# Kernel tuning notes

Measured on AMD Instinct MI355X. Metric: run time of the kernel, lower is better.

The kernel has to match this reference:

```python
import jax, jax.numpy as jnp
import numpy as np
import math

LOG2 = math.log(2.0)

def shifted_softplus(x):
    return jax.nn.softplus(x) - LOG2

def setup_inputs() -> dict:
    key = jax.random.key(0)
    ks = jax.random.split(key, 12)
    n_atoms, n_pairs = 40000, 640000
    d_basis, d_filt, n_rbf = 128, 128, 20
    x = jax.random.normal(ks[0], (n_atoms, d_basis), dtype=jnp.float32)
    f_ij = jax.random.uniform(ks[1], (n_pairs, n_rbf), dtype=jnp.float32)
    idx_i = jax.random.randint(ks[2], (n_pairs,), 0, n_atoms)
    idx_j = jax.random.randint(ks[3], (n_pairs,), 0, n_atoms)
    rcut_ij = jax.random.uniform(ks[4], (n_pairs,), dtype=jnp.float32)
    s_in = 1.0 / math.sqrt(d_basis)
    s_f = 1.0 / math.sqrt(n_rbf)
    s_out = 1.0 / math.sqrt(d_filt)
    W_in = jax.random.uniform(ks[5], (d_filt, d_basis), minval=-s_in, maxval=s_in)
    b_in = jax.random.uniform(ks[6], (d_filt,), minval=-s_in, maxval=s_in)
    W_f = jax.random.uniform(ks[7], (d_filt, n_rbf), minval=-s_f, maxval=s_f)
    b_f = jax.random.uniform(ks[8], (d_filt,), minval=-s_f, maxval=s_f)
    W_out = jax.random.uniform(ks[9], (d_basis, d_filt), minval=-s_out, maxval=s_out)
    b_out = jax.random.uniform(ks[10], (d_basis,), minval=-s_out, maxval=s_out)
    return {"x": x, "f_ij": f_ij, "idx_i": idx_i, "idx_j": idx_j, "rcut_ij": rcut_ij,
            "W_in": W_in, "b_in": b_in, "W_f": W_f, "b_f": b_f, "W_out": W_out, "b_out": b_out}

def reference(x, f_ij, idx_i, idx_j, rcut_ij, W_in, b_in, W_f, b_f, W_out, b_out):
    n_atoms = x.shape[0]
    # input_to_feature: Linear(d_basis -> d_filt)
    h = x @ W_in.T + b_in                                  # [n_atoms, d_filt]
    # filter_network: Linear(n_rbf -> d_filt) + ShiftedSoftplus, scaled by cutoff
    Wij = shifted_softplus(f_ij @ W_f.T + b_f) * rcut_ij[:, None]  # [n_pairs, d_filt]
    # gather neighbor features, modulate, scatter-add back to atoms
    x_ij = h[idx_j] * Wij                                  # [n_pairs, d_filt]
    agg = jax.ops.segment_sum(x_ij, idx_i, num_segments=n_atoms)   # [n_atoms, d_filt]
    # feature_to_output: Linear(d_filt -> d_basis) + ShiftedSoftplus
    return shifted_softplus(agg @ W_out.T + b_out)
```

## Files before the change

### kernel.cpp

```cpp
#include <hip/hip_runtime.h>
#include <hip/hip_bf16.h>
#include <hip/hip_fp16.h>

typedef __hip_bfloat16 bf16;
typedef __attribute__((ext_vector_type(8))) short short8;
typedef __attribute__((ext_vector_type(4))) float f32x4;

__device__ __forceinline__ float braw2f(unsigned short u) {
    return __uint_as_float(((unsigned int)u) << 16);
}
__device__ __forceinline__ unsigned short f2braw(float f) {
    bf16 b = __float2bfloat16(f);
    return *(unsigned short*)&b;
}
__device__ __forceinline__ unsigned int pack2(float lo, float hi) {
    return (unsigned int)f2braw(lo) | ((unsigned int)f2braw(hi) << 16);
}
__device__ __forceinline__ float h2f(unsigned short u) {
    __half h = *(__half*)&u;
    return __half2float(h);
}

#define LN2F 0.69314718055994531f
__device__ __forceinline__ float ssp(float x) {
    return fmaxf(x, 0.0f) + __logf(1.0f + __expf(-fabsf(x))) - LN2F;
}

template<bool ACT, bool OUT_BF16>
__global__ __launch_bounds__(256) void linear128_mfma_kernel(
    const float* __restrict__ X, const float* __restrict__ W, const float* __restrict__ Bias,
    void* __restrict__ Yv, int n_rows)
{
    __shared__ unsigned short wls[128 * 128];
    __shared__ unsigned short xs[64 * 128];
    __shared__ float bls[128];

    const float4* W4 = (const float4*)W;
    for (int i = threadIdx.x; i < 128 * 32; i += 256) {
        float4 w = W4[i];
        ushort4 s; s.x = f2braw(w.x); s.y = f2braw(w.y); s.z = f2braw(w.z); s.w = f2braw(w.w);
        *(ushort4*)&wls[i * 4] = s;
    }
    if (threadIdx.x < 128) bls[threadIdx.x] = Bias[threadIdx.x];

    const int base = blockIdx.x * 64;
    const float4* X4 = (const float4*)X;
    for (int i = threadIdx.x; i < 64 * 32; i += 256) {
        int r = i >> 5, k4 = i & 31;
        int row = base + r;
        float4 v = (row < n_rows) ? X4[(size_t)row * 32 + k4] : make_float4(0.f, 0.f, 0.f, 0.f);
        ushort4 s; s.x = f2braw(v.x); s.y = f2braw(v.y); s.z = f2braw(v.z); s.w = f2braw(v.w);
        *(ushort4*)&xs[r * 128 + k4 * 4] = s;
    }
    __syncthreads();

    const int wv = threadIdx.x >> 6;
    const int l  = threadIdx.x & 63;
    const int lm = l & 15;
    const int lq = l >> 4;

    short8 a[4];
    #pragma unroll
    for (int kk = 0; kk < 4; ++kk)
        a[kk] = *(const short8*)&xs[(wv * 16 + lm) * 128 + kk * 32 + lq * 8];

    f32x4 acc[8];
    #pragma unroll
    for (int ct = 0; ct < 8; ++ct) {
        f32x4 c = {0.f, 0.f, 0.f, 0.f};
        #pragma unroll
        for (int kk = 0; kk < 4; ++kk) {
            short8 b = *(const short8*)&wls[(ct * 16 + lm) * 128 + kk * 32 + lq * 8];
            c = __builtin_amdgcn_mfma_f32_16x16x32_bf16(a[kk], b, c, 0, 0, 0);
        }
        acc[ct] = c;
    }

    #pragma unroll
    for (int ct = 0; ct < 8; ++ct) {
        int col = ct * 16 + lm;
        float bia = bls[col];
        #pragma unroll
        for (int r = 0; r < 4; ++r) {
            int row = base + wv * 16 + lq * 4 + r;
            if (row < n_rows) {
                float o = acc[ct][r] + bia;
                if (ACT) o = ssp(o);
                if (OUT_BF16) ((unsigned short*)Yv)[(size_t)row * 128 + col] = f2braw(o);
                else          ((float*)Yv)[(size_t)row * 128 + col] = o;
            }
        }
    }
}


__global__ __launch_bounds__(256) void zero_int_kernel(int* __restrict__ p, int n) {
    int i = blockIdx.x * 256 + threadIdx.x;
    if (i < n) p[i] = 0;
}

__global__ __launch_bounds__(256) void hist_kernel(
    const int* __restrict__ idx_i, int* __restrict__ cnt, int n_pairs, int n_atoms)
{
    for (int p = blockIdx.x * 256 + threadIdx.x; p < n_pairs; p += gridDim.x * 256) {
        int ai = idx_i[p];
        if ((unsigned)ai < (unsigned)n_atoms) atomicAdd(&cnt[ai], 1);
    }
}

__global__ __launch_bounds__(1024) void scan1_kernel(
    const int* __restrict__ cnt, int* __restrict__ offs, int* __restrict__ partials, int n)
{
    __shared__ int sm[1024];
    int t = threadIdx.x, idx = blockIdx.x * 1024 + t;
    int v = (idx < n) ? cnt[idx] : 0;
    sm[t] = v;
    __syncthreads();
    #pragma unroll
    for (int d = 1; d < 1024; d <<= 1) {
        int tmp = (t >= d) ? sm[t - d] : 0;
        __syncthreads();
        sm[t] += tmp;
        __syncthreads();
    }
    if (idx < n) offs[idx] = sm[t] - v;
    if (t == 1023) partials[blockIdx.x] = sm[1023];
}

__global__ __launch_bounds__(64) void scan2_kernel(
    int* __restrict__ partials, int* __restrict__ offs, int nb, int n)
{
    __shared__ int sm[64];
    int t = threadIdx.x;
    int v = (t < nb) ? partials[t] : 0;
    sm[t] = v;
    __syncthreads();
    #pragma unroll
    for (int d = 1; d < 64; d <<= 1) {
        int tmp = (t >= d) ? sm[t - d] : 0;
        __syncthreads();
        sm[t] += tmp;
        __syncthreads();
    }
    if (t < nb) partials[t] = sm[t] - v;
    if (t == 63) offs[n] = sm[63];
}

__global__ __launch_bounds__(1024) void scan3_kernel(
    int* __restrict__ offs, int* __restrict__ cur, const int* __restrict__ partials, int n)
{
    int idx = blockIdx.x * 1024 + threadIdx.x;
    if (idx < n) {
        int o = offs[idx] + partials[blockIdx.x];
        offs[idx] = o;
        cur[idx] = o;
    }
}

template<bool WRITE_ATOM>
__global__ __launch_bounds__(256) void scatter_pay_kernel(
    const float* __restrict__ f_ij, const int* __restrict__ idx_i, const int* __restrict__ idx_j,
    const float* __restrict__ rcut, int* __restrict__ cur, uint4* __restrict__ pay,
    int* __restrict__ pair_atom, int n_pairs, int n_atoms)
{
    if (blockIdx.x == 0 && threadIdx.x < 204) {
        ((int*)(pay + (size_t)n_pairs * 3))[threadIdx.x] = 0;
    }
    for (int p = blockIdx.x * 256 + threadIdx.x; p < n_pairs; p += gridDim.x * 256) {
        int ai = idx_i[p];
        if ((unsigned)ai >= (unsigned)n_atoms) continue;
        int pos = atomicAdd(&cur[ai], 1);
        const float4* fr = (const float4*)(f_ij + (size_t)p * 20);
        float4 f0 = fr[0], f1 = fr[1], f2 = fr[2], f3 = fr[3], f4 = fr[4];
        uint4 q0, q1, q2;
        q0.x = pack2(f0.x, f0.y); q0.y = pack2(f0.z, f0.w);
        q0.z = pack2(f1.x, f1.y); q0.w = pack2(f1.z, f1.w);
        q1.x = pack2(f2.x, f2.y); q1.y = pack2(f2.z, f2.w);
        q1.z = pack2(f3.x, f3.y); q1.w = pack2(f3.z, f3.w);
        q2.x = pack2(f4.x, f4.y); q2.y = pack2(f4.z, f4.w);
        q2.z = (unsigned int)idx_j[p];
        q2.w = __float_as_uint(rcut[p]);
        uint4* dst = pay + (size_t)pos * 3;
        dst[0] = q0; dst[1] = q1; dst[2] = q2;
        if (WRITE_ATOM) pair_atom[pos] = ai;
    }
}

__global__ __launch_bounds__(256) void fused_pair_kernel(
    const uint4* __restrict__ pay, const int* __restrict__ pair_atom,
    const float* __restrict__ W_f, const float* __restrict__ b_f,
    const unsigned int* __restrict__ hb32, float* __restrict__ agg, int n_pairs)
{
    __shared__ unsigned short wls[128 * 40];
    __shared__ float bls[128];
    __shared__ unsigned short wij[64 * 132];
    __shared__ int lds_atom[64];
    __shared__ int lds_aj[64];

    for (int i = threadIdx.x; i < 128 * 32; i += 256) {
        int col = i >> 5, k = i & 31;
        float v = (k < 20) ? W_f[col * 20 + k] : 0.f;
        wls[col * 40 + k] = f2braw(v);
    }
    if (threadIdx.x < 128) bls[threadIdx.x] = b_f[threadIdx.x];

    const int P0 = blockIdx.x * 64;
    if (threadIdx.x < 64) {
        int p = P0 + threadIdx.x;
        bool valid = p < n_pairs;
        lds_atom[threadIdx.x] = valid ? pair_atom[p] : -1;
        lds_aj[threadIdx.x]   = valid ? (int)((const unsigned int*)pay)[(size_t)p * 12 + 10] : 0;
    }
    __syncthreads();

    const int wv = threadIdx.x >> 6;
    const int l  = threadIdx.x & 63;
    const int lm = l & 15;
    const int lq = l >> 4;
    const int p0 = P0 + wv * 16;

    if (p0 < n_pairs) {
        const char* rec = (const char*)pay + (size_t)(p0 + lm) * 48;
        short8 a = *(const short8*)(rec + lq * 16);
        if (lq == 2) { a[4] = 0; a[5] = 0; a[6] = 0; a[7] = 0; }
        if (lq == 3) { a[0]=0; a[1]=0; a[2]=0; a[3]=0; a[4]=0; a[5]=0; a[6]=0; a[7]=0; }

        f32x4 acc[8];
        #pragma unroll
        for (int ct = 0; ct < 8; ++ct) {
            short8 b = *(const short8*)&wls[(ct * 16 + lm) * 40 + lq * 8];
            f32x4 z = {0.f, 0.f, 0.f, 0.f};
            acc[ct] = __builtin_amdgcn_mfma_f32_16x16x32_bf16(a, b, z, 0, 0, 0);
        }

        float rc[4];
        #pragma unroll
        for (int r = 0; r < 4; ++r) {
            int p = p0 + lq * 4 + r;
            rc[r] = (p < n_pairs) ? ((const float*)pay)[(size_t)p * 12 + 11] : 0.f;
        }
        #pragma unroll
        for (int ct = 0; ct < 8; ++ct) {
            float bia = bls[ct * 16 + lm];
            #pragma unroll
            for (int r = 0; r < 4; ++r) {
                float o = ssp(acc[ct][r] + bia) * rc[r];
                __half hh = __float2half(o);
                wij[(wv * 16 + lq * 4 + r) * 132 + ct * 16 + lm] = *(unsigned short*)&hh;
            }
        }
    }
    __syncthreads();

    int nv = n_pairs - p0;
    if (nv > 16) nv = 16;
    if (nv > 0) {
        float a0 = 0.f, a1 = 0.f;
        int cura = lds_atom[wv * 16];
        #pragma unroll 4
        for (int k = 0; k < nv; ++k) {
            int pa = lds_atom[wv * 16 + k];
            if (pa != cura) {
                atomicAdd(&agg[(size_t)cura * 128 + 2 * l], a0);
                atomicAdd(&agg[(size_t)cura * 128 + 2 * l + 1], a1);
                a0 = 0.f; a1 = 0.f; cura = pa;
            }
            int aj = lds_aj[wv * 16 + k];
            unsigned int h = hb32[(size_t)aj * 64 + l];
            unsigned int w = *(const unsigned int*)&wij[(wv * 16 + k) * 132 + 2 * l];
            a0 += __uint_as_float(h << 16) * h2f((unsigned short)(w & 0xffffu));
            a1 += __uint_as_float(h & 0xffff0000u) * h2f((unsigned short)(w >> 16));
        }
        atomicAdd(&agg[(size_t)cura * 128 + 2 * l], a0);
        atomicAdd(&agg[(size_t)cura * 128 + 2 * l + 1], a1);
    }
}

__global__ __launch_bounds__(256) void segment_pay_kernel(
    const uint4* __restrict__ pay, const float* __restrict__ W_f,
    const float* __restrict__ b_f, const unsigned int* __restrict__ hb32,
    const int* __restrict__ offs, float* __restrict__ agg, int n_atoms)
{
    const int wave = (blockIdx.x * 256 + threadIdx.x) >> 6;
    const int lane = threadIdx.x & 63;
    if (wave >= n_atoms) return;

    const int c0 = 2 * lane;
    float w0[20], w1[20];
    #pragma unroll
    for (int r = 0; r < 20; ++r) {
        w0[r] = W_f[c0 * 20 + r];
        w1[r] = W_f[(c0 + 1) * 20 + r];
    }
    const float b0 = b_f[c0], b1 = b_f[c0 + 1];

    const int cs = offs[wave], ce = offs[wave + 1];
    float acc0 = 0.f, acc1 = 0.f;

    int s = cs;
    for (; s + 2 <= ce; s += 2) {
        const uint4* pA = pay + (size_t)s * 3;
        const uint4* pB = pA + 3;
        uint4 qA0 = pA[0], qA1 = pA[1], qA2 = pA[2];
        uint4 qB0 = pB[0], qB1 = pB[1], qB2 = pB[2];
        unsigned int uA[10] = {qA0.x,qA0.y,qA0.z,qA0.w,qA1.x,qA1.y,qA1.z,qA1.w,qA2.x,qA2.y};
        unsigned int uB[10] = {qB0.x,qB0.y,qB0.z,qB0.w,qB1.x,qB1.y,qB1.z,qB1.w,qB2.x,qB2.y};
        float a0A = b0, a1A = b1, a0B = b0, a1B = b1;
        #pragma unroll
        for (int r = 0; r < 10; ++r) {
            float loA = __uint_as_float(uA[r] << 16);
            float hiA = __uint_as_float(uA[r] & 0xffff0000u);
            float loB = __uint_as_float(uB[r] << 16);
            float hiB = __uint_as_float(uB[r] & 0xffff0000u);
            a0A += loA * w0[2*r];     a1A += loA * w1[2*r];
            a0A += hiA * w0[2*r + 1]; a1A += hiA * w1[2*r + 1];
            a0B += loB * w0[2*r];     a1B += loB * w1[2*r];
            a0B += hiB * w0[2*r + 1]; a1B += hiB * w1[2*r + 1];
        }
        float rcA = __uint_as_float(qA2.w), rcB = __uint_as_float(qB2.w);
        float wv0A = ssp(a0A) * rcA, wv1A = ssp(a1A) * rcA;
        float wv0B = ssp(a0B) * rcB, wv1B = ssp(a1B) * rcB;
        unsigned int hA = hb32[(size_t)(int)qA2.z * 64 + lane];
        unsigned int hB = hb32[(size_t)(int)qB2.z * 64 + lane];
        acc0 += __uint_as_float(hA << 16) * wv0A + __uint_as_float(hB << 16) * wv0B;
        acc1 += __uint_as_float(hA & 0xffff0000u) * wv1A + __uint_as_float(hB & 0xffff0000u) * wv1B;
    }
    if (s < ce) {
        const uint4* pA = pay + (size_t)s * 3;
        uint4 q0 = pA[0], q1 = pA[1], q2 = pA[2];
        unsigned int u[10] = {q0.x,q0.y,q0.z,q0.w,q1.x,q1.y,q1.z,q1.w,q2.x,q2.y};
        float a0 = b0, a1 = b1;
        #pragma unroll
        for (int r = 0; r < 10; ++r) {
            float lo = __uint_as_float(u[r] << 16);
            float hi = __uint_as_float(u[r] & 0xffff0000u);
            a0 += lo * w0[2*r];     a1 += lo * w1[2*r];
            a0 += hi * w0[2*r + 1]; a1 += hi * w1[2*r + 1];
        }
        float rc = __uint_as_float(q2.w);
        float wv0 = ssp(a0) * rc, wv1 = ssp(a1) * rc;
        unsigned int h = hb32[(size_t)(int)q2.z * 64 + lane];
        acc0 += __uint_as_float(h << 16) * wv0;
        acc1 += __uint_as_float(h & 0xffff0000u) * wv1;
    }

    *(float2*)&agg[(size_t)wave * 128 + c0] = make_float2(acc0, acc1);
}

__global__ __launch_bounds__(256) void scatter_kernel(
    const int* __restrict__ idx_i, int* __restrict__ cur, int* __restrict__ perm,
    int n_pairs, int n_atoms)
{
    for (int p = blockIdx.x * 256 + threadIdx.x; p < n_pairs; p += gridDim.x * 256) {
        int ai = idx_i[p];
        if ((unsigned)ai < (unsigned)n_atoms) {
            int pos = atomicAdd(&cur[ai], 1);
            perm[pos] = p;
        }
    }
}

__global__ __launch_bounds__(256) void segment_kernel(
    const float* __restrict__ f_ij, const int* __restrict__ idx_j,
    const float* __restrict__ rcut, const float* __restrict__ W_f,
    const float* __restrict__ b_f, const unsigned short* __restrict__ hb,
    const int* __restrict__ offs, const int* __restrict__ perm,
    float* __restrict__ agg, int n_atoms)
{
    const int wave = (blockIdx.x * 256 + threadIdx.x) >> 6;
    const int lane = threadIdx.x & 63;
    if (wave >= n_atoms) return;

    float w0[20], w1[20];
    #pragma unroll
    for (int r = 0; r < 20; ++r) {
        w0[r] = W_f[lane * 20 + r];
        w1[r] = W_f[(lane + 64) * 20 + r];
    }
    const float b0 = b_f[lane], b1 = b_f[lane + 64];

    const int cs = offs[wave], ce = offs[wave + 1];
    float acc0 = 0.f, acc1 = 0.f;

    int s = cs;
    for (; s + 2 <= ce; s += 2) {
        int pA = perm[s], pB = perm[s + 1];
        int ajA = idx_j[pA], ajB = idx_j[pB];
        float rcA = rcut[pA], rcB = rcut[pB];
        const float4* frA = (const float4*)(f_ij + (size_t)pA * 20);
        const float4* frB = (const float4*)(f_ij + (size_t)pB * 20);
        float a0A = b0, a1A = b1, a0B = b0, a1B = b1;
        #pragma unroll
        for (int q = 0; q < 5; ++q) {
            float4 fA = frA[q], fB = frB[q];
            a0A += fA.x * w0[4*q+0]; a1A += fA.x * w1[4*q+0];
            a0A += fA.y * w0[4*q+1]; a1A += fA.y * w1[4*q+1];
            a0A += fA.z * w0[4*q+2]; a1A += fA.z * w1[4*q+2];
            a0A += fA.w * w0[4*q+3]; a1A += fA.w * w1[4*q+3];
            a0B += fB.x * w0[4*q+0]; a1B += fB.x * w1[4*q+0];
            a0B += fB.y * w0[4*q+1]; a1B += fB.y * w1[4*q+1];
            a0B += fB.z * w0[4*q+2]; a1B += fB.z * w1[4*q+2];
            a0B += fB.w * w0[4*q+3]; a1B += fB.w * w1[4*q+3];
        }
        float wv0A = ssp(a0A) * rcA, wv1A = ssp(a1A) * rcA;
        float wv0B = ssp(a0B) * rcB, wv1B = ssp(a1B) * rcB;
        float h0A = braw2f(hb[(size_t)ajA * 128 + lane]);
        float h1A = braw2f(hb[(size_t)ajA * 128 + 64 + lane]);
        float h0B = braw2f(hb[(size_t)ajB * 128 + lane]);
        float h1B = braw2f(hb[(size_t)ajB * 128 + 64 + lane]);
        acc0 += h0A * wv0A + h0B * wv0B;
        acc1 += h1A * wv1A + h1B * wv1B;
    }
    if (s < ce) {
        int p = perm[s];
        int aj = idx_j[p];
        float rc = rcut[p];
        const float4* fr = (const float4*)(f_ij + (size_t)p * 20);
        float a0 = b0, a1 = b1;
        #pragma unroll
        for (int q = 0; q < 5; ++q) {
            float4 fv = fr[q];
            a0 += fv.x * w0[4*q+0]; a1 += fv.x * w1[4*q+0];
            a0 += fv.y * w0[4*q+1]; a1 += fv.y * w1[4*q+1];
            a0 += fv.z * w0[4*q+2]; a1 += fv.z * w1[4*q+2];
            a0 += fv.w * w0[4*q+3]; a1 += fv.w * w1[4*q+3];
        }
        float wv0 = ssp(a0) * rc, wv1 = ssp(a1) * rc;
        acc0 += braw2f(hb[(size_t)aj * 128 + lane]) * wv0;
        acc1 += braw2f(hb[(size_t)aj * 128 + 64 + lane]) * wv1;
    }

    agg[(size_t)wave * 128 + lane]      = acc0;
    agg[(size_t)wave * 128 + 64 + lane] = acc1;
}

static inline size_t align_up(size_t v, size_t a) { return (v + a - 1) & ~(a - 1); }

extern "C" void kernel_launch(void* const* d_in, const int* in_sizes, int n_in,
                              void* d_out, int out_size, void* d_ws, size_t ws_size,
                              hipStream_t stream) {
    const float* x     = (const float*)d_in[0];
    const float* f_ij  = (const float*)d_in[1];
    const int*   idx_i = (const int*)d_in[2];
    const int*   idx_j = (const int*)d_in[3];
    const float* rcut  = (const float*)d_in[4];
    const float* W_in  = (const float*)d_in[5];
    const float* b_in  = (const float*)d_in[6];
    const float* W_f   = (const float*)d_in[7];
    const float* b_f   = (const float*)d_in[8];
    const float* W_out = (const float*)d_in[9];
    const float* b_out = (const float*)d_in[10];

    const int n_atoms = in_sizes[0] / 128;
    const int n_pairs = in_sizes[2];
    const int nscan = (n_atoms + 1023) / 1024;
    const int mfma_grid = (n_atoms + 63) / 64;

    size_t off_hb   = 0;
    size_t off_offs = align_up(off_hb + (size_t)n_atoms * 128 * 2, 16);
    size_t off_cur  = align_up(off_offs + (size_t)(n_atoms + 1) * 4, 16);
    size_t off_part = align_up(off_cur + (size_t)n_atoms * 4, 16);
    size_t off_pay  = align_up(off_part + (size_t)nscan * 4, 64);
    size_t need_pay = off_pay + (size_t)n_pairs * 48;
    size_t off_pa   = align_up(off_pay + (size_t)n_pairs * 48 + 816, 256);
    size_t need_fused = off_pa + (size_t)(n_pairs + 64) * 4;

    if (ws_size >= need_fused) {
        unsigned short* hb  = (unsigned short*)((char*)d_ws + off_hb);
        int*   offs = (int*)((char*)d_ws + off_offs);
        int*   cur  = (int*)((char*)d_ws + off_cur);
        int*   part = (int*)((char*)d_ws + off_part);
        uint4* pay  = (uint4*)((char*)d_ws + off_pay);
        int*   pair_atom = (int*)((char*)d_ws + off_pa);
        float* agg = (float*)d_out;

        linear128_mfma_kernel<false, true><<<dim3(mfma_grid), dim3(256), 0, stream>>>(
            x, W_in, b_in, (void*)hb, n_atoms);

        zero_int_kernel<<<dim3((n_atoms * 128 + 255) / 256), dim3(256), 0, stream>>>(
            (int*)agg, n_atoms * 128);

        zero_int_kernel<<<dim3((n_atoms + 255) / 256), dim3(256), 0, stream>>>(cur, n_atoms);
        hist_kernel<<<dim3(1024), dim3(256), 0, stream>>>(idx_i, cur, n_pairs, n_atoms);
        scan1_kernel<<<dim3(nscan), dim3(1024), 0, stream>>>(cur, offs, part, n_atoms);
        scan2_kernel<<<dim3(1), dim3(64), 0, stream>>>(part, offs, nscan, n_atoms);
        scan3_kernel<<<dim3(nscan), dim3(1024), 0, stream>>>(offs, cur, part, n_atoms);
        scatter_pay_kernel<true><<<dim3(1024), dim3(256), 0, stream>>>(
            f_ij, idx_i, idx_j, rcut, cur, pay, pair_atom, n_pairs, n_atoms);

        fused_pair_kernel<<<dim3((n_pairs + 63) / 64), dim3(256), 0, stream>>>(
            pay, pair_atom, W_f, b_f, (const unsigned int*)hb, agg, n_pairs);

        linear128_mfma_kernel<true, false><<<dim3(mfma_grid), dim3(256), 0, stream>>>(
            agg, W_out, b_out, d_out, n_atoms);
    } else if (ws_size >= need_pay) {
        unsigned short* hb = (unsigned short*)((char*)d_ws + off_hb);
        int*  offs = (int*)((char*)d_ws + off_offs);
        int*  cur  = (int*)((char*)d_ws + off_cur);
        int*  part = (int*)((char*)d_ws + off_part);
        uint4* pay = (uint4*)((char*)d_ws + off_pay);
        float* agg = (float*)d_out;

        linear128_mfma_kernel<false, true><<<dim3(mfma_grid), dim3(256), 0, stream>>>(
            x, W_in, b_in, (void*)hb, n_atoms);

        zero_int_kernel<<<dim3((n_atoms + 255) / 256), dim3(256), 0, stream>>>(cur, n_atoms);
        hist_kernel<<<dim3(1024), dim3(256), 0, stream>>>(idx_i, cur, n_pairs, n_atoms);
        scan1_kernel<<<dim3(nscan), dim3(1024), 0, stream>>>(cur, offs, part, n_atoms);
        scan2_kernel<<<dim3(1), dim3(64), 0, stream>>>(part, offs, nscan, n_atoms);
        scan3_kernel<<<dim3(nscan), dim3(1024), 0, stream>>>(offs, cur, part, n_atoms);
        scatter_pay_kernel<false><<<dim3(1024), dim3(256), 0, stream>>>(
            f_ij, idx_i, idx_j, rcut, cur, pay, (int*)nullptr, n_pairs, n_atoms);

        segment_pay_kernel<<<dim3((n_atoms + 3) / 4), dim3(256), 0, stream>>>(
            pay, W_f, b_f, (const unsigned int*)hb, offs, agg, n_atoms);

        linear128_mfma_kernel<true, false><<<dim3(mfma_grid), dim3(256), 0, stream>>>(
            agg, W_out, b_out, d_out, n_atoms);
    } else {
        size_t o_h    = 0;
        size_t o_offs = o_h + (size_t)n_atoms * 128 * 2;
        size_t o_cur  = o_offs + (size_t)(n_atoms + 1) * 4;
        size_t o_perm = o_cur + (size_t)n_atoms * 4;
        size_t o_part = o_perm + (size_t)n_pairs * 4;
        unsigned short* hb = (unsigned short*)((char*)d_ws + o_h);
        int* offs = (int*)((char*)d_ws + o_offs);
        int* cur  = (int*)((char*)d_ws + o_cur);
        int* perm = (int*)((char*)d_ws + o_perm);
        int* part = (int*)((char*)d_ws + o_part);
        float* agg = (float*)d_out;

        linear128_mfma_kernel<false, true><<<dim3(mfma_grid), dim3(256), 0, stream>>>(
            x, W_in, b_in, (void*)hb, n_atoms);

        zero_int_kernel<<<dim3((n_atoms + 255) / 256), dim3(256), 0, stream>>>(cur, n_atoms);
        hist_kernel<<<dim3(1024), dim3(256), 0, stream>>>(idx_i, cur, n_pairs, n_atoms);
        scan1_kernel<<<dim3(nscan), dim3(1024), 0, stream>>>(cur, offs, part, n_atoms);
        scan2_kernel<<<dim3(1), dim3(64), 0, stream>>>(part, offs, nscan, n_atoms);
        scan3_kernel<<<dim3(nscan), dim3(1024), 0, stream>>>(offs, cur, part, n_atoms);
        scatter_kernel<<<dim3(1024), dim3(256), 0, stream>>>(idx_i, cur, perm, n_pairs, n_atoms);

        segment_kernel<<<dim3((n_atoms + 3) / 4), dim3(256), 0, stream>>>(
            f_ij, idx_j, rcut, W_f, b_f, hb, offs, perm, agg, n_atoms);

        linear128_mfma_kernel<true, false><<<dim3(mfma_grid), dim3(256), 0, stream>>>(
            agg, W_out, b_out, d_out, n_atoms);
    }
}
```

Before: 377.4 us.

## Make fused pair kernel loop over four 16-pair chunks per wave without block barriers

Each wave now handles 64 consecutive sorted pairs in four 16-pair chunks, using per-wave LDS buffers instead of block-wide barriers. Its running per-atom accumulator carries across chunks, so fewer atomics are issued at segment boundaries. The W_f staging into LDS is amortized over four times fewer blocks. The two zeroing launches are merged into one kernel. Without a wave barrier between chunk iterations, there is a possible LDS write-after-read hazard, although lockstep wave execution likely makes it safe.

```diff
diff --git a/kernel.cpp b/kernel.cpp
--- a/kernel.cpp
+++ b/kernel.cpp
@@ -97,6 +97,15 @@
 __global__ __launch_bounds__(256) void zero_int_kernel(int* __restrict__ p, int n) {
     int i = blockIdx.x * 256 + threadIdx.x;
     if (i < n) p[i] = 0;
+}
+
+__global__ __launch_bounds__(256) void zero2_kernel(
+    int* __restrict__ a, int na, int* __restrict__ b, int nb)
+{
+    int i = blockIdx.x * 256 + threadIdx.x;
+    if (i < na) a[i] = 0;
+    int j = i - na;
+    if (j >= 0 && j < nb) b[j] = 0;
 }
 
 __global__ __launch_bounds__(256) void hist_kernel(
@@ -186,6 +195,8 @@
     }
 }
 
+#define FP_NITER 4
+
 __global__ __launch_bounds__(256) void fused_pair_kernel(
     const uint4* __restrict__ pay, const int* __restrict__ pair_atom,
     const float* __restrict__ W_f, const float* __restrict__ b_f,
@@ -193,9 +204,9 @@
 {
     __shared__ unsigned short wls[128 * 40];
     __shared__ float bls[128];
-    __shared__ unsigned short wij[64 * 132];
-    __shared__ int lds_atom[64];
-    __shared__ int lds_aj[64];
+    __shared__ unsigned short wij[4][16 * 132];
+    __shared__ int lds_atom[4][16];
+    __shared__ int lds_aj[4][16];
 
     for (int i = threadIdx.x; i < 128 * 32; i += 256) {
         int col = i >> 5, k = i & 31;
@@ -203,23 +214,28 @@
         wls[col * 40 + k] = f2braw(v);
     }
     if (threadIdx.x < 128) bls[threadIdx.x] = b_f[threadIdx.x];
-
-    const int P0 = blockIdx.x * 64;
-    if (threadIdx.x < 64) {
-        int p = P0 + threadIdx.x;
-        bool valid = p < n_pairs;
-        lds_atom[threadIdx.x] = valid ? pair_atom[p] : -1;
-        lds_aj[threadIdx.x]   = valid ? (int)((const unsigned int*)pay)[(size_t)p * 12 + 10] : 0;
-    }
     __syncthreads();
 
     const int wv = threadIdx.x >> 6;
     const int l  = threadIdx.x & 63;
     const int lm = l & 15;
     const int lq = l >> 4;
-    const int p0 = P0 + wv * 16;
-
-    if (p0 < n_pairs) {
+
+    const int base = (blockIdx.x * 4 + wv) * (16 * FP_NITER);
+    float a0 = 0.f, a1 = 0.f;
+    int cura = -1;
+
+    for (int t = 0; t < FP_NITER; ++t) {
+        const int p0 = base + t * 16;
+        if (p0 >= n_pairs) break;
+
+        if (l < 16) {
+            int p = p0 + l;
+            bool valid = p < n_pairs;
+            lds_atom[wv][l] = valid ? pair_atom[p] : -1;
+            lds_aj[wv][l]   = valid ? (int)((const unsigned int*)pay)[(size_t)p * 12 + 10] : 0;
+        }
+
         const char* rec = (const char*)pay + (size_t)(p0 + lm) * 48;
         short8 a = *(const short8*)(rec + lq * 16);
         if (lq == 2) { a[4] = 0; a[5] = 0; a[6] = 0; a[7] = 0; }
@@ -246,31 +262,32 @@
             for (int r = 0; r < 4; ++r) {
                 float o = ssp(acc[ct][r] + bia) * rc[r];
                 __half hh = __float2half(o);
-                wij[(wv * 16 + lq * 4 + r) * 132 + ct * 16 + lm] = *(unsigned short*)&hh;
+                wij[wv][(lq * 4 + r) * 132 + ct * 16 + lm] = *(unsigned short*)&hh;
             }
         }
-    }
-    __syncthreads();
-
-    int nv = n_pairs - p0;
-    if (nv > 16) nv = 16;
-    if (nv > 0) {
-        float a0 = 0.f, a1 = 0.f;
-        int cura = lds_atom[wv * 16];
+
+        asm volatile("s_waitcnt lgkmcnt(0)" ::: "memory");
+
+        int nv = n_pairs - p0;
+        if (nv > 16) nv = 16;
         #pragma unroll 4
         for (int k = 0; k < nv; ++k) {
-            int pa = lds_atom[wv * 16 + k];
+            int pa = lds_atom[wv][k];
             if (pa != cura) {
-                atomicAdd(&agg[(size_t)cura * 128 + 2 * l], a0);
-                atomicAdd(&agg[(size_t)cura * 128 + 2 * l + 1], a1);
+                if (cura >= 0) {
+                    atomicAdd(&agg[(size_t)cura * 128 + 2 * l], a0);
+                    atomicAdd(&agg[(size_t)cura * 128 + 2 * l + 1], a1);
+                }
                 a0 = 0.f; a1 = 0.f; cura = pa;
             }
-            int aj = lds_aj[wv * 16 + k];
+            int aj = lds_aj[wv][k];
             unsigned int h = hb32[(size_t)aj * 64 + l];
-            unsigned int w = *(const unsigned int*)&wij[(wv * 16 + k) * 132 + 2 * l];
+            unsigned int w = *(const unsigned int*)&wij[wv][k * 132 + 2 * l];
             a0 += __uint_as_float(h << 16) * h2f((unsigned short)(w & 0xffffu));
             a1 += __uint_as_float(h & 0xffff0000u) * h2f((unsigned short)(w >> 16));
         }
+    }
+    if (cura >= 0) {
         atomicAdd(&agg[(size_t)cura * 128 + 2 * l], a0);
         atomicAdd(&agg[(size_t)cura * 128 + 2 * l + 1], a1);
     }
@@ -477,10 +494,9 @@
         linear128_mfma_kernel<false, true><<<dim3(mfma_grid), dim3(256), 0, stream>>>(
             x, W_in, b_in, (void*)hb, n_atoms);
 
-        zero_int_kernel<<<dim3((n_atoms * 128 + 255) / 256), dim3(256), 0, stream>>>(
-            (int*)agg, n_atoms * 128);
-
-        zero_int_kernel<<<dim3((n_atoms + 255) / 256), dim3(256), 0, stream>>>(cur, n_atoms);
+        zero2_kernel<<<dim3((n_atoms * 128 + n_atoms + 255) / 256), dim3(256), 0, stream>>>(
+            (int*)agg, n_atoms * 128, cur, n_atoms);
+
         hist_kernel<<<dim3(1024), dim3(256), 0, stream>>>(idx_i, cur, n_pairs, n_atoms);
         scan1_kernel<<<dim3(nscan), dim3(1024), 0, stream>>>(cur, offs, part, n_atoms);
         scan2_kernel<<<dim3(1), dim3(64), 0, stream>>>(part, offs, nscan, n_atoms);
@@ -488,7 +504,8 @@
         scatter_pay_kernel<true><<<dim3(1024), dim3(256), 0, stream>>>(
             f_ij, idx_i, idx_j, rcut, cur, pay, pair_atom, n_pairs, n_atoms);
 
-        fused_pair_kernel<<<dim3((n_pairs + 63) / 64), dim3(256), 0, stream>>>(
+        int fp_blocks = (n_pairs + 64 * FP_NITER - 1) / (64 * FP_NITER);
+        fused_pair_kernel<<<dim3(fp_blocks), dim3(256), 0, stream>>>(
             pay, pair_atom, W_f, b_f, (const unsigned int*)hb, agg, n_pairs);
 
         linear128_mfma_kernel<true, false><<<dim3(mfma_grid), dim3(256), 0, stream>>>(
```

New measurement: 368.6 us. 1.02x faster.
